# Kernel tuning notes

Hardware: AMD Instinct MI355X
Metric: run time of the kernel (lower is better)

Reference implementation:

```python
import jax, jax.numpy as jnp
import numpy as np

N_HEADS = 16
HEAD_DIM = 64
SEQ_LEN = 2048
BATCH = 1


def alibi_slopes(n_heads):
    start = 2.0 ** (-8.0 / n_heads)
    return jnp.asarray([start * start ** i for i in range(n_heads)], dtype=jnp.float32)


def setup_inputs() -> dict:
    key = jax.random.key(0)
    kq, kk, kv = jax.random.split(key, 3)
    shape = (BATCH, N_HEADS, SEQ_LEN, HEAD_DIM)
    return {
        "q": jax.random.normal(kq, shape, dtype=jnp.float32),
        "k": jax.random.normal(kk, shape, dtype=jnp.float32),
        "v": jax.random.normal(kv, shape, dtype=jnp.float32),
    }


def reference(q, k, v):
    # q,k,v: [B,H,S,D]
    seq_len = q.shape[2]
    head_dim = q.shape[3]
    scale = 1.0 / np.sqrt(head_dim).astype(np.float32)
    # scores: [B,H,S,S]
    scores = jnp.einsum("bhsd,bhtd->bhst", q, k) * scale
    pos = jnp.arange(seq_len)
    # distances[i, j] = j - i  (pos.unsqueeze(0) - pos.unsqueeze(1))
    distances = (pos[None, :] - pos[:, None]).astype(jnp.float32)  # [S,S]
    slopes = alibi_slopes(q.shape[1])  # [H]
    alibi = slopes[:, None, None] * distances[None, :, :]  # [H,S,S]
    scores = scores + alibi[None]
    attn = jax.nn.softmax(scores, axis=-1)
    return jnp.einsum("bhst,bhtd->bhsd", attn, v)
```

## Files before the change

kernel.cpp:

```cpp
#include <hip/hip_runtime.h>
#include <hip/hip_bf16.h>
#include <stdint.h>

#define N_HEADS 16
#define HEAD_DIM 64
#define SEQ_LEN 2048
#define KVBLK 32
#define HALF_LEN (SEQ_LEN / 2)
#define NTILES (HALF_LEN / KVBLK)

typedef __bf16 bf16x8 __attribute__((ext_vector_type(8)));
typedef __bf16 bf16x4 __attribute__((ext_vector_type(4)));
typedef short  s16x4  __attribute__((ext_vector_type(4)));
typedef float  f32x4  __attribute__((ext_vector_type(4)));
typedef unsigned int u32x4 __attribute__((ext_vector_type(4)));

#if __has_builtin(__builtin_amdgcn_mfma_f32_16x16x16bf16_1k)
#define HAVE_MFMA16 1
#else
#define HAVE_MFMA16 0
#endif

static __device__ __forceinline__ unsigned pkbf(float a, float b) {
    union { __bf16 h[2]; unsigned u; } t;
    t.h[0] = (__bf16)a; t.h[1] = (__bf16)b;
    return t.u;
}

__global__ __launch_bounds__(512, 4)
void attn_alibi_kernel(const float* __restrict__ q,
                       const float* __restrict__ k,
                       const float* __restrict__ v,
                       float* __restrict__ out) {
    const int tid  = threadIdx.x;
    const int wave = tid >> 6;
    const int lane = tid & 63;
    const int col  = lane & 15;
    const int g    = lane >> 4;
    const int half = wave >> 2;
    const int w4   = wave & 3;

    const int h      = blockIdx.y;
    const int qbase  = blockIdx.x * 64 + w4 * 16;
    const int kstart = half * HALF_LEN;

    const float* qh = q + (size_t)h * SEQ_LEN * HEAD_DIM;
    const float* kh = k + (size_t)h * SEQ_LEN * HEAD_DIM;
    const float* vh = v + (size_t)h * SEQ_LEN * HEAD_DIM;
    float*       oh = out + (size_t)h * SEQ_LEN * HEAD_DIM;

    __shared__ alignas(16) char smem[32768];
    char* kbase  = smem + half * 8192;
    char* vtbase = smem + 16384 + half * 8192;

    const float LOG2E  = 1.4426950408889634f;
    const float scale2 = 0.125f * LOG2E;
    const float slope  = exp2f(-0.5f * (float)(h + 1));
    const float slope2 = slope * LOG2E;

    bf16x8 qf[2];
    {
        const float* qr = qh + (size_t)(qbase + col) * HEAD_DIM + g * 8;
        #pragma unroll
        for (int c = 0; c < 2; ++c)
            #pragma unroll
            for (int b = 0; b < 8; ++b) qf[c][b] = (__bf16)qr[c * 32 + b];
    }

    float cb[2][4];
    #pragma unroll
    for (int jt = 0; jt < 2; ++jt)
        #pragma unroll
        for (int r = 0; r < 4; ++r)
            cb[jt][r] = slope2 * (float)(jt * 16 + g * 4 + r - (qbase + col));

    float m = -1e30f, l = 0.0f;
    f32x4 acc[4];
    #pragma unroll
    for (int dt = 0; dt < 4; ++dt) acc[dt] = (f32x4)0.0f;

    const int hid  = tid & 255;
    const int krow = hid >> 3;
    const int kcol = (hid & 7) * 8;
    const float* ksrc = kh + (size_t)(kstart + krow) * HEAD_DIM + kcol;
    char* kdst = kbase + krow * 128 + ((kcol * 2) ^ ((krow & 7) << 4));

    const int vc = hid & 63;
    const int vr = (hid >> 6) * 8;
    const float* vsrc = vh + (size_t)(kstart + vr) * HEAD_DIM + vc;
    char* vtdst = vtbase + (((vc * 64) + (vr * 2)) ^ ((vc & 7) << 4));

    f32x4 kr0, kr1;
    float vv[8];

    kr0 = *(const f32x4*)(ksrc);
    kr1 = *(const f32x4*)(ksrc + 4);
    #pragma unroll
    for (int j = 0; j < 8; ++j) vv[j] = vsrc[(size_t)j * HEAD_DIM];
    {
        bf16x8 kb16, vb16;
        #pragma unroll
        for (int b = 0; b < 4; ++b) { kb16[b] = (__bf16)kr0[b]; kb16[4 + b] = (__bf16)kr1[b]; }
        #pragma unroll
        for (int j = 0; j < 8; ++j) vb16[j] = (__bf16)vv[j];
        *(bf16x8*)(kdst)  = kb16;
        *(bf16x8*)(vtdst) = vb16;
    }
    __syncthreads();

    for (int t = 0; t < NTILES; ++t) {
        const int kb  = kstart + t * KVBLK;
        const int buf = t & 1;
        const char* kbuf  = kbase + buf * 4096;
        const char* vtbuf = vtbase + buf * 4096;

        f32x4 sacc[2];
        sacc[0] = (f32x4)0.0f;
        sacc[1] = (f32x4)0.0f;
        #pragma unroll
        for (int jt = 0; jt < 2; ++jt) {
            const int row = jt * 16 + col;
            #pragma unroll
            for (int c = 0; c < 2; ++c) {
                bf16x8 kf = *(const bf16x8*)(kbuf + row * 128
                                             + ((c * 64 + g * 16) ^ ((row & 7) << 4)));
                sacc[jt] = __builtin_amdgcn_mfma_f32_16x16x32_bf16(kf, qf[c], sacc[jt], 0, 0, 0);
            }
        }

        if (t + 1 < NTILES) {
            const float* ks = ksrc + (size_t)(t + 1) * KVBLK * HEAD_DIM;
            const float* vs = vsrc + (size_t)(t + 1) * KVBLK * HEAD_DIM;
            kr0 = *(const f32x4*)(ks);
            kr1 = *(const f32x4*)(ks + 4);
            #pragma unroll
            for (int j = 0; j < 8; ++j) vv[j] = vs[(size_t)j * HEAD_DIM];
        }

        const float skb = slope2 * (float)kb;
        float s[2][4];
        #pragma unroll
        for (int jt = 0; jt < 2; ++jt)
            #pragma unroll
            for (int r = 0; r < 4; ++r)
                s[jt][r] = sacc[jt][r] * scale2 + (cb[jt][r] + skb);

        float x = s[0][0];
        #pragma unroll
        for (int jt = 0; jt < 2; ++jt)
            #pragma unroll
            for (int r = 0; r < 4; ++r) x = fmaxf(x, s[jt][r]);
        x = fmaxf(x, __shfl_xor(x, 16));
        x = fmaxf(x, __shfl_xor(x, 32));
        float mn    = fmaxf(m, x);
        float alpha = __builtin_amdgcn_exp2f(m - mn);
        m = mn;
        float p[2][4], y = 0.0f;
        #pragma unroll
        for (int jt = 0; jt < 2; ++jt)
            #pragma unroll
            for (int r = 0; r < 4; ++r) {
                p[jt][r] = __builtin_amdgcn_exp2f(s[jt][r] - mn);
                y += p[jt][r];
            }
        y += __shfl_xor(y, 16);
        y += __shfl_xor(y, 32);
        l = l * alpha + y;
        #pragma unroll
        for (int dt = 0; dt < 4; ++dt) acc[dt] *= alpha;

#if HAVE_MFMA16
        bf16x4 pf0, pf1;
        #pragma unroll
        for (int b = 0; b < 4; ++b) { pf0[b] = (__bf16)p[0][b]; pf1[b] = (__bf16)p[1][b]; }
        const s16x4 pb0 = __builtin_bit_cast(s16x4, pf0);
        const s16x4 pb1 = __builtin_bit_cast(s16x4, pf1);
        #pragma unroll
        for (int dt = 0; dt < 4; ++dt) {
            const int vrow = dt * 16 + col;
            const int rb   = vrow * 64;
            const int swz  = (vrow & 7) << 4;
            bf16x4 vf0 = *(const bf16x4*)(vtbuf + ((rb + g * 8) ^ swz));
            bf16x4 vf1 = *(const bf16x4*)(vtbuf + ((rb + 32 + g * 8) ^ swz));
            acc[dt] = __builtin_amdgcn_mfma_f32_16x16x16bf16_1k(
                __builtin_bit_cast(s16x4, vf0), pb0, acc[dt], 0, 0, 0);
            acc[dt] = __builtin_amdgcn_mfma_f32_16x16x16bf16_1k(
                __builtin_bit_cast(s16x4, vf1), pb1, acc[dt], 0, 0, 0);
        }
#else
        unsigned pk00 = pkbf(p[0][0], p[0][1]);
        unsigned pk01 = pkbf(p[0][2], p[0][3]);
        unsigned pk10 = pkbf(p[1][0], p[1][1]);
        unsigned pk11 = pkbf(p[1][2], p[1][3]);
        const int srcA = col + ((g & 1) << 5);
        const int srcB = srcA + 16;
        unsigned a00 = __shfl(pk00, srcA), a01 = __shfl(pk01, srcA);
        unsigned a10 = __shfl(pk10, srcA), a11 = __shfl(pk11, srcA);
        unsigned b00 = __shfl(pk00, srcB), b01 = __shfl(pk01, srcB);
        unsigned b10 = __shfl(pk10, srcB), b11 = __shfl(pk11, srcB);
        const bool hi = g >= 2;
        u32x4 pu;
        pu[0] = hi ? a10 : a00;
        pu[1] = hi ? a11 : a01;
        pu[2] = hi ? b10 : b00;
        pu[3] = hi ? b11 : b01;
        bf16x8 pf = __builtin_bit_cast(bf16x8, pu);
        #pragma unroll
        for (int dt = 0; dt < 4; ++dt) {
            const int vrow = dt * 16 + col;
            bf16x8 vf = *(const bf16x8*)(vtbuf
                            + ((vrow * 64 + g * 16) ^ ((vrow & 7) << 4)));
            acc[dt] = __builtin_amdgcn_mfma_f32_16x16x32_bf16(vf, pf, acc[dt], 0, 0, 0);
        }
#endif

        if (t + 1 < NTILES) {
            bf16x8 kb16, vb16;
            #pragma unroll
            for (int b = 0; b < 4; ++b) { kb16[b] = (__bf16)kr0[b]; kb16[4 + b] = (__bf16)kr1[b]; }
            #pragma unroll
            for (int j = 0; j < 8; ++j) vb16[j] = (__bf16)vv[j];
            *(bf16x8*)(kdst  + ((t + 1) & 1) * 4096) = kb16;
            *(bf16x8*)(vtdst + ((t + 1) & 1) * 4096) = vb16;
        }
        __syncthreads();
    }

    float* eacc = (float*)smem;
    float* eml  = (float*)(smem + 16384);

    if (half == 1) {
        #pragma unroll
        for (int dt = 0; dt < 4; ++dt)
            *(f32x4*)(eacc + w4 * 1024 + col * 64 + dt * 16 + g * 4) = acc[dt];
        if (g == 0) {
            eml[(w4 * 16 + col) * 2 + 0] = m;
            eml[(w4 * 16 + col) * 2 + 1] = l;
        }
    }
    __syncthreads();
    if (half == 0) {
        float m2 = eml[(w4 * 16 + col) * 2 + 0];
        float l2 = eml[(w4 * 16 + col) * 2 + 1];
        float mm = fmaxf(m, m2);
        float a1 = __builtin_amdgcn_exp2f(m - mm);
        float a2 = __builtin_amdgcn_exp2f(m2 - mm);
        float inv = 1.0f / (l * a1 + l2 * a2);
        float* orow = oh + (size_t)(qbase + col) * HEAD_DIM;
        #pragma unroll
        for (int dt = 0; dt < 4; ++dt) {
            f32x4 o2 = *(const f32x4*)(eacc + w4 * 1024 + col * 64 + dt * 16 + g * 4);
            f32x4 res = (acc[dt] * a1 + o2 * a2) * inv;
            *(f32x4*)(orow + dt * 16 + g * 4) = res;
        }
    }
}

extern "C" void kernel_launch(void* const* d_in, const int* in_sizes, int n_in,
                              void* d_out, int out_size, void* d_ws, size_t ws_size,
                              hipStream_t stream) {
    const float* q = (const float*)d_in[0];
    const float* k = (const float*)d_in[1];
    const float* v = (const float*)d_in[2];
    float* out = (float*)d_out;

    dim3 grid(SEQ_LEN / 64, N_HEADS, 1);
    dim3 block(512, 1, 1);
    attn_alibi_kernel<<<grid, block, 0, stream>>>(q, k, v, out);
}
```

Baseline: 52.05 us.

## Split KV range across four wave groups with 1024-thread blocks

```diff
diff --git a/kernel.cpp b/kernel.cpp
--- a/kernel.cpp
+++ b/kernel.cpp
@@ -6,8 +6,8 @@
 #define HEAD_DIM 64
 #define SEQ_LEN 2048
 #define KVBLK 32
-#define HALF_LEN (SEQ_LEN / 2)
-#define NTILES (HALF_LEN / KVBLK)
+#define QTR_LEN (SEQ_LEN / 4)
+#define NTILES (QTR_LEN / KVBLK)
 
 typedef __bf16 bf16x8 __attribute__((ext_vector_type(8)));
 typedef __bf16 bf16x4 __attribute__((ext_vector_type(4)));
@@ -27,7 +27,7 @@
     return t.u;
 }
 
-__global__ __launch_bounds__(512, 4)
+__global__ __launch_bounds__(1024, 8)
 void attn_alibi_kernel(const float* __restrict__ q,
                        const float* __restrict__ k,
                        const float* __restrict__ v,
@@ -37,21 +37,21 @@
     const int lane = tid & 63;
     const int col  = lane & 15;
     const int g    = lane >> 4;
-    const int half = wave >> 2;
+    const int qtr  = wave >> 2;
     const int w4   = wave & 3;
 
     const int h      = blockIdx.y;
     const int qbase  = blockIdx.x * 64 + w4 * 16;
-    const int kstart = half * HALF_LEN;
+    const int kstart = qtr * QTR_LEN;
 
     const float* qh = q + (size_t)h * SEQ_LEN * HEAD_DIM;
     const float* kh = k + (size_t)h * SEQ_LEN * HEAD_DIM;
     const float* vh = v + (size_t)h * SEQ_LEN * HEAD_DIM;
     float*       oh = out + (size_t)h * SEQ_LEN * HEAD_DIM;
 
-    __shared__ alignas(16) char smem[32768];
-    char* kbase  = smem + half * 8192;
-    char* vtbase = smem + 16384 + half * 8192;
+    __shared__ alignas(16) char smem[65536];
+    char* kbase  = smem + qtr * 8192;
+    char* vtbase = smem + 32768 + qtr * 8192;
 
     const float LOG2E  = 1.4426950408889634f;
     const float scale2 = 0.125f * LOG2E;
@@ -227,31 +227,45 @@
     }
 
     float* eacc = (float*)smem;
-    float* eml  = (float*)(smem + 16384);
-
-    if (half == 1) {
+    float* eml  = (float*)(smem + 49152);
+
+    if (qtr != 0) {
+        float* ea = eacc + (qtr - 1) * 4096 + w4 * 1024 + col * 64;
         #pragma unroll
         for (int dt = 0; dt < 4; ++dt)
-            *(f32x4*)(eacc + w4 * 1024 + col * 64 + dt * 16 + g * 4) = acc[dt];
+            *(f32x4*)(ea + dt * 16 + g * 4) = acc[dt];
         if (g == 0) {
-            eml[(w4 * 16 + col) * 2 + 0] = m;
-            eml[(w4 * 16 + col) * 2 + 1] = l;
+            eml[((qtr - 1) * 64 + w4 * 16 + col) * 2 + 0] = m;
+            eml[((qtr - 1) * 64 + w4 * 16 + col) * 2 + 1] = l;
         }
     }
     __syncthreads();
-    if (half == 0) {
-        float m2 = eml[(w4 * 16 + col) * 2 + 0];
-        float l2 = eml[(w4 * 16 + col) * 2 + 1];
-        float mm = fmaxf(m, m2);
-        float a1 = __builtin_amdgcn_exp2f(m - mm);
-        float a2 = __builtin_amdgcn_exp2f(m2 - mm);
-        float inv = 1.0f / (l * a1 + l2 * a2);
+    if (qtr == 0) {
+        float mi[3], li[3];
+        float mm = m;
+        #pragma unroll
+        for (int i = 0; i < 3; ++i) {
+            mi[i] = eml[(i * 64 + w4 * 16 + col) * 2 + 0];
+            li[i] = eml[(i * 64 + w4 * 16 + col) * 2 + 1];
+            mm = fmaxf(mm, mi[i]);
+        }
+        float a0 = __builtin_amdgcn_exp2f(m - mm);
+        float lt = l * a0;
+        float ai[3];
+        #pragma unroll
+        for (int i = 0; i < 3; ++i) {
+            ai[i] = __builtin_amdgcn_exp2f(mi[i] - mm);
+            lt += li[i] * ai[i];
+        }
+        float inv = 1.0f / lt;
         float* orow = oh + (size_t)(qbase + col) * HEAD_DIM;
         #pragma unroll
         for (int dt = 0; dt < 4; ++dt) {
-            f32x4 o2 = *(const f32x4*)(eacc + w4 * 1024 + col * 64 + dt * 16 + g * 4);
-            f32x4 res = (acc[dt] * a1 + o2 * a2) * inv;
-            *(f32x4*)(orow + dt * 16 + g * 4) = res;
+            f32x4 o = acc[dt] * a0;
+            #pragma unroll
+            for (int i = 0; i < 3; ++i)
+                o += *(const f32x4*)(eacc + i * 4096 + w4 * 1024 + col * 64 + dt * 16 + g * 4) * ai[i];
+            *(f32x4*)(orow + dt * 16 + g * 4) = o * inv;
         }
     }
 }
@@ -265,6 +279,6 @@
     float* out = (float*)d_out;
 
     dim3 grid(SEQ_LEN / 64, N_HEADS, 1);
-    dim3 block(512, 1, 1);
+    dim3 block(1024, 1, 1);
     attn_alibi_kernel<<<grid, block, 0, stream>>>(q, k, v, out);
 }
```

Result: slower. 138.0 us (+165.1%).

## Split KV range across grid z and merge partial softmax results

Applied to the files above, without the earlier changes.

```diff
diff --git a/kernel.cpp b/kernel.cpp
--- a/kernel.cpp
+++ b/kernel.cpp
@@ -6,8 +6,6 @@
 #define HEAD_DIM 64
 #define SEQ_LEN 2048
 #define KVBLK 32
-#define HALF_LEN (SEQ_LEN / 2)
-#define NTILES (HALF_LEN / KVBLK)
 
 typedef __bf16 bf16x8 __attribute__((ext_vector_type(8)));
 typedef __bf16 bf16x4 __attribute__((ext_vector_type(4)));
@@ -27,11 +25,14 @@
     return t.u;
 }
 
+template <int NT, bool PARTIAL>
 __global__ __launch_bounds__(512, 4)
 void attn_alibi_kernel(const float* __restrict__ q,
                        const float* __restrict__ k,
                        const float* __restrict__ v,
-                       float* __restrict__ out) {
+                       float* __restrict__ out,
+                       float* __restrict__ wsO,
+                       float* __restrict__ wsML) {
     const int tid  = threadIdx.x;
     const int wave = tid >> 6;
     const int lane = tid & 63;
@@ -42,12 +43,11 @@
 
     const int h      = blockIdx.y;
     const int qbase  = blockIdx.x * 64 + w4 * 16;
-    const int kstart = half * HALF_LEN;
+    const int kstart = blockIdx.z * (2 * NT * KVBLK) + half * (NT * KVBLK);
 
     const float* qh = q + (size_t)h * SEQ_LEN * HEAD_DIM;
     const float* kh = k + (size_t)h * SEQ_LEN * HEAD_DIM;
     const float* vh = v + (size_t)h * SEQ_LEN * HEAD_DIM;
-    float*       oh = out + (size_t)h * SEQ_LEN * HEAD_DIM;
 
     __shared__ alignas(16) char smem[32768];
     char* kbase  = smem + half * 8192;
@@ -108,7 +108,7 @@
     }
     __syncthreads();
 
-    for (int t = 0; t < NTILES; ++t) {
+    for (int t = 0; t < NT; ++t) {
         const int kb  = kstart + t * KVBLK;
         const int buf = t & 1;
         const char* kbuf  = kbase + buf * 4096;
@@ -128,7 +128,7 @@
             }
         }
 
-        if (t + 1 < NTILES) {
+        if (t + 1 < NT) {
             const float* ks = ksrc + (size_t)(t + 1) * KVBLK * HEAD_DIM;
             const float* vs = vsrc + (size_t)(t + 1) * KVBLK * HEAD_DIM;
             kr0 = *(const f32x4*)(ks);
@@ -214,7 +214,7 @@
         }
 #endif
 
-        if (t + 1 < NTILES) {
+        if (t + 1 < NT) {
             bf16x8 kb16, vb16;
             #pragma unroll
             for (int b = 0; b < 4; ++b) { kb16[b] = (__bf16)kr0[b]; kb16[4 + b] = (__bf16)kr1[b]; }
@@ -245,15 +245,54 @@
         float mm = fmaxf(m, m2);
         float a1 = __builtin_amdgcn_exp2f(m - mm);
         float a2 = __builtin_amdgcn_exp2f(m2 - mm);
-        float inv = 1.0f / (l * a1 + l2 * a2);
-        float* orow = oh + (size_t)(qbase + col) * HEAD_DIM;
-        #pragma unroll
-        for (int dt = 0; dt < 4; ++dt) {
-            f32x4 o2 = *(const f32x4*)(eacc + w4 * 1024 + col * 64 + dt * 16 + g * 4);
-            f32x4 res = (acc[dt] * a1 + o2 * a2) * inv;
-            *(f32x4*)(orow + dt * 16 + g * 4) = res;
-        }
-    }
+        float lt = l * a1 + l2 * a2;
+
+        if (PARTIAL) {
+            const size_t zrow = (size_t)blockIdx.z * (N_HEADS * SEQ_LEN)
+                              + (size_t)h * SEQ_LEN + qbase + col;
+            float* orow = wsO + zrow * HEAD_DIM;
+            #pragma unroll
+            for (int dt = 0; dt < 4; ++dt) {
+                f32x4 o2 = *(const f32x4*)(eacc + w4 * 1024 + col * 64 + dt * 16 + g * 4);
+                *(f32x4*)(orow + dt * 16 + g * 4) = acc[dt] * a1 + o2 * a2;
+            }
+            if (g == 0) {
+                wsML[zrow * 2 + 0] = mm;
+                wsML[zrow * 2 + 1] = lt;
+            }
+        } else {
+            float inv = 1.0f / lt;
+            float* orow = out + ((size_t)h * SEQ_LEN + qbase + col) * HEAD_DIM;
+            #pragma unroll
+            for (int dt = 0; dt < 4; ++dt) {
+                f32x4 o2 = *(const f32x4*)(eacc + w4 * 1024 + col * 64 + dt * 16 + g * 4);
+                *(f32x4*)(orow + dt * 16 + g * 4) = (acc[dt] * a1 + o2 * a2) * inv;
+            }
+        }
+    }
+}
+
+__global__ __launch_bounds__(256)
+void merge_kernel(const float* __restrict__ wsO,
+                  const float* __restrict__ wsML,
+                  float* __restrict__ out) {
+    const int idx  = blockIdx.x * 256 + threadIdx.x;
+    const int row  = idx >> 4;
+    const int quad = idx & 15;
+    const int NROW = N_HEADS * SEQ_LEN;
+
+    float m0 = wsML[(size_t)row * 2 + 0];
+    float l0 = wsML[(size_t)row * 2 + 1];
+    float m1 = wsML[((size_t)NROW + row) * 2 + 0];
+    float l1 = wsML[((size_t)NROW + row) * 2 + 1];
+    float mm = fmaxf(m0, m1);
+    float a0 = __builtin_amdgcn_exp2f(m0 - mm);
+    float a1 = __builtin_amdgcn_exp2f(m1 - mm);
+    float inv = 1.0f / (l0 * a0 + l1 * a1);
+
+    f32x4 o0 = *(const f32x4*)(wsO + (size_t)row * HEAD_DIM + quad * 4);
+    f32x4 o1 = *(const f32x4*)(wsO + ((size_t)NROW + row) * HEAD_DIM + quad * 4);
+    *(f32x4*)(out + (size_t)row * HEAD_DIM + quad * 4) = (o0 * a0 + o1 * a1) * inv;
 }
 
 extern "C" void kernel_launch(void* const* d_in, const int* in_sizes, int n_in,
@@ -264,7 +303,20 @@
     const float* v = (const float*)d_in[2];
     float* out = (float*)d_out;
 
-    dim3 grid(SEQ_LEN / 64, N_HEADS, 1);
-    dim3 block(512, 1, 1);
-    attn_alibi_kernel<<<grid, block, 0, stream>>>(q, k, v, out);
+    const size_t nO  = (size_t)2 * N_HEADS * SEQ_LEN * HEAD_DIM;
+    const size_t nML = (size_t)2 * N_HEADS * SEQ_LEN * 2;
+    const size_t need = (nO + nML) * sizeof(float);
+
+    if (ws_size >= need) {
+        float* wsO  = (float*)d_ws;
+        float* wsML = wsO + nO;
+        dim3 grid(SEQ_LEN / 64, N_HEADS, 2);
+        attn_alibi_kernel<16, true><<<grid, dim3(512, 1, 1), 0, stream>>>(
+            q, k, v, out, wsO, wsML);
+        merge_kernel<<<dim3(2048, 1, 1), dim3(256, 1, 1), 0, stream>>>(wsO, wsML, out);
+    } else {
+        dim3 grid(SEQ_LEN / 64, N_HEADS, 1);
+        attn_alibi_kernel<32, false><<<grid, dim3(512, 1, 1), 0, stream>>>(
+            q, k, v, out, nullptr, nullptr);
+    }
 }
```

Measured after the change: 59.38 us. 14.1% more time.

## Precompute swizzled bf16 K and transposed V tile images in a prep kernel

Applied to the files above, without the earlier changes.

```diff
diff --git a/kernel.cpp b/kernel.cpp
--- a/kernel.cpp
+++ b/kernel.cpp
@@ -6,8 +6,8 @@
 #define HEAD_DIM 64
 #define SEQ_LEN 2048
 #define KVBLK 32
-#define HALF_LEN (SEQ_LEN / 2)
-#define NTILES (HALF_LEN / KVBLK)
+#define NT 32
+#define NTILE_TOT (SEQ_LEN / KVBLK)
 
 typedef __bf16 bf16x8 __attribute__((ext_vector_type(8)));
 typedef __bf16 bf16x4 __attribute__((ext_vector_type(4)));
@@ -27,11 +27,44 @@
     return t.u;
 }
 
+__global__ __launch_bounds__(256)
+void prep_kernel(const float* __restrict__ k,
+                 const float* __restrict__ v,
+                 char* __restrict__ kimg,
+                 char* __restrict__ vtimg) {
+    const int ts  = blockIdx.x;
+    const int h   = blockIdx.y;
+    const int tid = threadIdx.x;
+    const int s0  = ts * KVBLK;
+    const size_t blk = ((size_t)h * NTILE_TOT + ts) * 4096;
+
+    const int krow = tid >> 3;
+    const int kcol = (tid & 7) * 8;
+    const float* ks = k + ((size_t)h * SEQ_LEN + s0 + krow) * HEAD_DIM + kcol;
+    f32x4 a = *(const f32x4*)ks;
+    f32x4 b = *(const f32x4*)(ks + 4);
+    bf16x8 kb;
+    #pragma unroll
+    for (int i = 0; i < 4; ++i) { kb[i] = (__bf16)a[i]; kb[4 + i] = (__bf16)b[i]; }
+    *(bf16x8*)(kimg + blk + krow * 128 + ((kcol * 2) ^ ((krow & 7) << 4))) = kb;
+
+    const int vc = tid & 63;
+    const int vr = (tid >> 6) * 8;
+    const float* vs = v + ((size_t)h * SEQ_LEN + s0 + vr) * HEAD_DIM + vc;
+    bf16x8 vb;
+    #pragma unroll
+    for (int j = 0; j < 8; ++j) vb[j] = (__bf16)vs[(size_t)j * HEAD_DIM];
+    *(bf16x8*)(vtimg + blk + (((vc * 64) + (vr * 2)) ^ ((vc & 7) << 4))) = vb;
+}
+
+template <bool IMG>
 __global__ __launch_bounds__(512, 4)
 void attn_alibi_kernel(const float* __restrict__ q,
                        const float* __restrict__ k,
                        const float* __restrict__ v,
-                       float* __restrict__ out) {
+                       float* __restrict__ out,
+                       const char* __restrict__ kimg,
+                       const char* __restrict__ vtimg) {
     const int tid  = threadIdx.x;
     const int wave = tid >> 6;
     const int lane = tid & 63;
@@ -42,12 +75,11 @@
 
     const int h      = blockIdx.y;
     const int qbase  = blockIdx.x * 64 + w4 * 16;
-    const int kstart = half * HALF_LEN;
+    const int kstart = half * (NT * KVBLK);
 
     const float* qh = q + (size_t)h * SEQ_LEN * HEAD_DIM;
     const float* kh = k + (size_t)h * SEQ_LEN * HEAD_DIM;
     const float* vh = v + (size_t)h * SEQ_LEN * HEAD_DIM;
-    float*       oh = out + (size_t)h * SEQ_LEN * HEAD_DIM;
 
     __shared__ alignas(16) char smem[32768];
     char* kbase  = smem + half * 8192;
@@ -82,22 +114,42 @@
     const int hid  = tid & 255;
     const int krow = hid >> 3;
     const int kcol = (hid & 7) * 8;
-    const float* ksrc = kh + (size_t)(kstart + krow) * HEAD_DIM + kcol;
-    char* kdst = kbase + krow * 128 + ((kcol * 2) ^ ((krow & 7) << 4));
-
-    const int vc = hid & 63;
-    const int vr = (hid >> 6) * 8;
-    const float* vsrc = vh + (size_t)(kstart + vr) * HEAD_DIM + vc;
-    char* vtdst = vtbase + (((vc * 64) + (vr * 2)) ^ ((vc & 7) << 4));
-
+    const int vc   = hid & 63;
+    const int vr   = (hid >> 6) * 8;
+
+    const char* kis = nullptr;
+    const char* vis = nullptr;
+    const float* ksrc = nullptr;
+    const float* vsrc = nullptr;
+    char* kdst  = nullptr;
+    char* vtdst = nullptr;
+    if constexpr (IMG) {
+        const size_t base = ((size_t)h * NTILE_TOT + half * NT) * 4096 + hid * 16;
+        kis = kimg + base;
+        vis = vtimg + base;
+        kdst  = kbase + hid * 16;
+        vtdst = vtbase + hid * 16;
+    } else {
+        ksrc  = kh + (size_t)(kstart + krow) * HEAD_DIM + kcol;
+        kdst  = kbase + krow * 128 + ((kcol * 2) ^ ((krow & 7) << 4));
+        vsrc  = vh + (size_t)(kstart + vr) * HEAD_DIM + vc;
+        vtdst = vtbase + (((vc * 64) + (vr * 2)) ^ ((vc & 7) << 4));
+    }
+
+    f32x4 kreg, vreg;
     f32x4 kr0, kr1;
     float vv[8];
 
-    kr0 = *(const f32x4*)(ksrc);
-    kr1 = *(const f32x4*)(ksrc + 4);
-    #pragma unroll
-    for (int j = 0; j < 8; ++j) vv[j] = vsrc[(size_t)j * HEAD_DIM];
-    {
+    if constexpr (IMG) {
+        kreg = *(const f32x4*)(kis);
+        vreg = *(const f32x4*)(vis);
+        *(f32x4*)(kdst)  = kreg;
+        *(f32x4*)(vtdst) = vreg;
+    } else {
+        kr0 = *(const f32x4*)(ksrc);
+        kr1 = *(const f32x4*)(ksrc + 4);
+        #pragma unroll
+        for (int j = 0; j < 8; ++j) vv[j] = vsrc[(size_t)j * HEAD_DIM];
         bf16x8 kb16, vb16;
         #pragma unroll
         for (int b = 0; b < 4; ++b) { kb16[b] = (__bf16)kr0[b]; kb16[4 + b] = (__bf16)kr1[b]; }
@@ -108,7 +160,7 @@
     }
     __syncthreads();
 
-    for (int t = 0; t < NTILES; ++t) {
+    for (int t = 0; t < NT; ++t) {
         const int kb  = kstart + t * KVBLK;
         const int buf = t & 1;
         const char* kbuf  = kbase + buf * 4096;
@@ -128,13 +180,18 @@
             }
         }
 
-        if (t + 1 < NTILES) {
-            const float* ks = ksrc + (size_t)(t + 1) * KVBLK * HEAD_DIM;
-            const float* vs = vsrc + (size_t)(t + 1) * KVBLK * HEAD_DIM;
-            kr0 = *(const f32x4*)(ks);
-            kr1 = *(const f32x4*)(ks + 4);
-            #pragma unroll
-            for (int j = 0; j < 8; ++j) vv[j] = vs[(size_t)j * HEAD_DIM];
+        if (t + 1 < NT) {
+            if constexpr (IMG) {
+                kreg = *(const f32x4*)(kis + (size_t)(t + 1) * 4096);
+                vreg = *(const f32x4*)(vis + (size_t)(t + 1) * 4096);
+            } else {
+                const float* ks = ksrc + (size_t)(t + 1) * KVBLK * HEAD_DIM;
+                const float* vs = vsrc + (size_t)(t + 1) * KVBLK * HEAD_DIM;
+                kr0 = *(const f32x4*)(ks);
+                kr1 = *(const f32x4*)(ks + 4);
+                #pragma unroll
+                for (int j = 0; j < 8; ++j) vv[j] = vs[(size_t)j * HEAD_DIM];
+            }
         }
 
         const float skb = slope2 * (float)kb;
@@ -214,14 +271,20 @@
         }
 #endif
 
-        if (t + 1 < NTILES) {
-            bf16x8 kb16, vb16;
-            #pragma unroll
-            for (int b = 0; b < 4; ++b) { kb16[b] = (__bf16)kr0[b]; kb16[4 + b] = (__bf16)kr1[b]; }
-            #pragma unroll
-            for (int j = 0; j < 8; ++j) vb16[j] = (__bf16)vv[j];
-            *(bf16x8*)(kdst  + ((t + 1) & 1) * 4096) = kb16;
-            *(bf16x8*)(vtdst + ((t + 1) & 1) * 4096) = vb16;
+        if (t + 1 < NT) {
+            const int nb = (t + 1) & 1;
+            if constexpr (IMG) {
+                *(f32x4*)(kdst  + nb * 4096) = kreg;
+                *(f32x4*)(vtdst + nb * 4096) = vreg;
+            } else {
+                bf16x8 kb16, vb16;
+                #pragma unroll
+                for (int b = 0; b < 4; ++b) { kb16[b] = (__bf16)kr0[b]; kb16[4 + b] = (__bf16)kr1[b]; }
+                #pragma unroll
+                for (int j = 0; j < 8; ++j) vb16[j] = (__bf16)vv[j];
+                *(bf16x8*)(kdst  + nb * 4096) = kb16;
+                *(bf16x8*)(vtdst + nb * 4096) = vb16;
+            }
         }
         __syncthreads();
     }
@@ -246,12 +309,11 @@
         float a1 = __builtin_amdgcn_exp2f(m - mm);
         float a2 = __builtin_amdgcn_exp2f(m2 - mm);
         float inv = 1.0f / (l * a1 + l2 * a2);
-        float* orow = oh + (size_t)(qbase + col) * HEAD_DIM;
+        float* orow = out + ((size_t)h * SEQ_LEN + qbase + col) * HEAD_DIM;
         #pragma unroll
         for (int dt = 0; dt < 4; ++dt) {
             f32x4 o2 = *(const f32x4*)(eacc + w4 * 1024 + col * 64 + dt * 16 + g * 4);
-            f32x4 res = (acc[dt] * a1 + o2 * a2) * inv;
-            *(f32x4*)(orow + dt * 16 + g * 4) = res;
+            *(f32x4*)(orow + dt * 16 + g * 4) = (acc[dt] * a1 + o2 * a2) * inv;
         }
     }
 }
@@ -264,7 +326,18 @@
     const float* v = (const float*)d_in[2];
     float* out = (float*)d_out;
 
+    const size_t imgBytes = (size_t)N_HEADS * NTILE_TOT * 4096;
+
     dim3 grid(SEQ_LEN / 64, N_HEADS, 1);
-    dim3 block(512, 1, 1);
-    attn_alibi_kernel<<<grid, block, 0, stream>>>(q, k, v, out);
+    if (ws_size >= 2 * imgBytes) {
+        char* kimg  = (char*)d_ws;
+        char* vtimg = kimg + imgBytes;
+        prep_kernel<<<dim3(NTILE_TOT, N_HEADS, 1), dim3(256, 1, 1), 0, stream>>>(
+            k, v, kimg, vtimg);
+        attn_alibi_kernel<true><<<grid, dim3(512, 1, 1), 0, stream>>>(
+            q, k, v, out, kimg, vtimg);
+    } else {
+        attn_alibi_kernel<false><<<grid, dim3(512, 1, 1), 0, stream>>>(
+            q, k, v, out, nullptr, nullptr);
+    }
 }
```

New measurement: 51.43 us. No clear change (-1.2%).
